# Performance work log

Hardware: AMD Instinct MI355X
Metric: run time of the kernel (lower is better)

The kernel has to match this reference:

```python
import jax, jax.numpy as jnp
import numpy as np

N = 100000
E = 3200000
NEG_SLOPE = 0.2


def setup_inputs() -> dict:
    key = jax.random.key(0)
    ks = jax.random.split(key, 12)
    x = jax.random.normal(ks[0], (N, 4), dtype=jnp.float32)
    edge_index = jax.random.randint(ks[1], (2, E), 0, N, dtype=jnp.int64)
    # GATConv(4, 16, heads=4): lin (no bias), att_src/att_dst [H, C], bias [H*C]
    W1 = jax.random.normal(ks[2], (4, 4 * 16), dtype=jnp.float32) * 0.5
    as1 = jax.random.normal(ks[3], (4, 16), dtype=jnp.float32) * 0.5
    ad1 = jax.random.normal(ks[4], (4, 16), dtype=jnp.float32) * 0.5
    b1 = jnp.zeros((64,), dtype=jnp.float32)
    # GATConv(64, 2, heads=4)
    W2 = jax.random.normal(ks[5], (64, 4 * 2), dtype=jnp.float32) * 0.125
    as2 = jax.random.normal(ks[6], (4, 2), dtype=jnp.float32) * 0.5
    ad2 = jax.random.normal(ks[7], (4, 2), dtype=jnp.float32) * 0.5
    b2 = jnp.zeros((8,), dtype=jnp.float32)
    # out head Linear(8, 1)
    Wout = jax.random.normal(ks[8], (8, 1), dtype=jnp.float32) * 0.35
    bout = jnp.zeros((1,), dtype=jnp.float32)
    return {"x": x, "edge_index": edge_index, "W1": W1, "as1": as1, "ad1": ad1,
            "b1": b1, "W2": W2, "as2": as2, "ad2": ad2, "b2": b2,
            "Wout": Wout, "bout": bout}


def gat_conv(x, ei, W, a_src, a_dst, b, H, C, n):
    # PyG GATConv (concat=True, negative_slope=0.2), self-loops already in ei
    xw = (x @ W).reshape(n, H, C)                      # [N, H, C]
    src, dst = ei[0], ei[1]
    alpha_s = jnp.einsum('nhc,hc->nh', xw, a_src)      # [N, H]
    alpha_d = jnp.einsum('nhc,hc->nh', xw, a_dst)      # [N, H]
    e = jax.nn.leaky_relu(alpha_s[src] + alpha_d[dst], NEG_SLOPE)  # [E, H]
    # segment softmax over incoming edges of each destination node
    m = jax.ops.segment_max(e, dst, num_segments=n)    # [N, H]
    e = jnp.exp(e - m[dst])
    denom = jax.ops.segment_sum(e, dst, num_segments=n)
    alpha = e / (denom[dst] + 1e-16)                   # [E, H]
    msg = xw[src] * alpha[:, :, None]                  # [E, H, C]
    out = jax.ops.segment_sum(msg, dst, num_segments=n)  # [N, H, C]
    return out.reshape(n, H * C) + b


def reference(x, edge_index, W1, as1, ad1, b1, W2, as2, ad2, b2, Wout, bout):
    n = x.shape[0]
    ar = jnp.arange(n, dtype=edge_index.dtype)
    ei = jnp.concatenate([edge_index, jnp.stack([ar, ar])], axis=1)  # add self-loops
    h = jax.nn.elu(gat_conv(x, ei, W1, as1, ad1, b1, 4, 16, n))       # [N, 64]
    h = jax.nn.elu(gat_conv(h, ei, W2, as2, ad2, b2, 4, 2, n))        # [N, 8]
    g = jnp.mean(h, axis=0, keepdims=True)  # global_mean_pool, batch all zeros -> [1, 8]
    return jax.nn.sigmoid(g @ Wout + bout)  # [1, 1]
```

## Files before the change

kernel.cpp:

```cpp
#include <hip/hip_runtime.h>
#include <hip/hip_fp8.h>

#define NEG 0.2f
#define BSZ 224
#define MAXBUK 512
#define NBIN 512

typedef float v2f __attribute__((ext_vector_type(2)));

__device__ __forceinline__ float lrelu(float x){ return fmaxf(x, NEG * x); }
__device__ __forceinline__ float elufast(float x){ return x > 0.0f ? x : __expf(x) - 1.0f; }
__device__ __forceinline__ float b2f(unsigned short b){ return __uint_as_float((unsigned)b << 16); }
__device__ __forceinline__ unsigned short f2b(float x){
    unsigned u = __float_as_uint(x);
    return (unsigned short)((u + 0x7FFFu + ((u >> 16) & 1u)) >> 16);
}

__device__ __forceinline__ void fma8(uint2 r, float w, v2f* acc){
    v2f w2 = {w, w};
    v2f f0 = __builtin_amdgcn_cvt_pk_f32_fp8(r.x, false);
    v2f f1 = __builtin_amdgcn_cvt_pk_f32_fp8(r.x, true);
    v2f f2 = __builtin_amdgcn_cvt_pk_f32_fp8(r.y, false);
    v2f f3 = __builtin_amdgcn_cvt_pk_f32_fp8(r.y, true);
    acc[0] = __builtin_elementwise_fma(f0, w2, acc[0]);
    acc[1] = __builtin_elementwise_fma(f1, w2, acc[1]);
    acc[2] = __builtin_elementwise_fma(f2, w2, acc[2]);
    acc[3] = __builtin_elementwise_fma(f3, w2, acc[3]);
}

__global__ void k_l1_node(const float* __restrict__ x, const float* __restrict__ W1,
                          const float* __restrict__ as1, const float* __restrict__ ad1,
                          unsigned char* __restrict__ xw1, uint2* __restrict__ asvb,
                          float* __restrict__ adv, int N){
    __shared__ float sW[256], sA[64], sD[64];
    int tid = threadIdx.x;
    sW[tid] = W1[tid];
    if (tid < 64){ sA[tid] = as1[tid]; sD[tid] = ad1[tid]; }
    __syncthreads();
    int i = blockIdx.x * 256 + tid;
    if (i >= N) return;
    float4 xv = ((const float4*)x)[i];
    float xw[64];
    #pragma unroll
    for (int j = 0; j < 64; j++)
        xw[j] = xv.x * sW[j] + xv.y * sW[64 + j] + xv.z * sW[128 + j] + xv.w * sW[192 + j];
    unsigned wv[16];
    #pragma unroll
    for (int j = 0; j < 16; j++){
        unsigned p = 0;
        p = __builtin_amdgcn_cvt_pk_fp8_f32(xw[4 * j],     xw[4 * j + 1], p, false);
        p = __builtin_amdgcn_cvt_pk_fp8_f32(xw[4 * j + 2], xw[4 * j + 3], p, true);
        wv[j] = p;
    }
    uint4* dp = (uint4*)(xw1 + (size_t)i * 64);
    dp[0] = make_uint4(wv[0],  wv[1],  wv[2],  wv[3]);
    dp[1] = make_uint4(wv[4],  wv[5],  wv[6],  wv[7]);
    dp[2] = make_uint4(wv[8],  wv[9],  wv[10], wv[11]);
    dp[3] = make_uint4(wv[12], wv[13], wv[14], wv[15]);
    float al[4];
    #pragma unroll
    for (int h = 0; h < 4; h++){
        float as_ = 0.f, ad_ = 0.f;
        #pragma unroll
        for (int c = 0; c < 16; c++){
            as_ += xw[h * 16 + c] * sA[h * 16 + c];
            ad_ += xw[h * 16 + c] * sD[h * 16 + c];
        }
        al[h] = as_;
        adv[i * 4 + h] = ad_;
    }
    asvb[i] = make_uint2((unsigned)f2b(al[0]) | ((unsigned)f2b(al[1]) << 16),
                         (unsigned)f2b(al[2]) | ((unsigned)f2b(al[3]) << 16));
}

__global__ void k_bcount(const int* __restrict__ dst, int* __restrict__ blkcnt,
                         int E, int chunksz, int nbuk){
    __shared__ int hist[MAXBUK];
    for (int b = threadIdx.x; b < nbuk; b += 256) hist[b] = 0;
    __syncthreads();
    int e0 = blockIdx.x * chunksz, e1 = min(E, e0 + chunksz);
    for (int e = e0 + threadIdx.x; e < e1; e += 256)
        atomicAdd(&hist[(unsigned)dst[e] / BSZ], 1);
    __syncthreads();
    for (int b = threadIdx.x; b < nbuk; b += 256)
        blkcnt[b * NBIN + blockIdx.x] = hist[b];
}

__global__ void k_scanA(int* __restrict__ blkcnt, int* __restrict__ btot){
    __shared__ int ts[256];
    int b = blockIdx.x, t = threadIdx.x;
    int base = b * NBIN + t * 2;
    int a0 = blkcnt[base], a1 = blkcnt[base + 1];
    int sum = a0 + a1;
    ts[t] = sum; __syncthreads();
    for (int s = 1; s < 256; s <<= 1){
        int tmp = (t >= s) ? ts[t - s] : 0;
        __syncthreads();
        ts[t] += tmp;
        __syncthreads();
    }
    int excl = ts[t] - sum;
    blkcnt[base] = excl;
    blkcnt[base + 1] = excl + a0;
    if (t == 255) btot[b] = ts[255];
}

__global__ void k_scanB(const int* __restrict__ btot, int* __restrict__ bstart, int nbuk){
    __shared__ int ts[512];
    int t = threadIdx.x;
    int v = (t < nbuk) ? btot[t] : 0;
    int orig = v;
    ts[t] = v; __syncthreads();
    for (int s = 1; s < 512; s <<= 1){
        int tmp = (t >= s) ? ts[t - s] : 0;
        __syncthreads();
        ts[t] += tmp;
        __syncthreads();
    }
    if (t < nbuk) bstart[t] = ts[t] - orig;
    if (t == 511) bstart[nbuk] = ts[511];
}

__global__ void k_bin(const int* __restrict__ src, const int* __restrict__ dst,
                      const int* __restrict__ blkcnt, const int* __restrict__ bstart,
                      unsigned* __restrict__ staged, int E, int chunksz, int nbuk){
    __shared__ int cur[MAXBUK];
    for (int b = threadIdx.x; b < nbuk; b += 256)
        cur[b] = bstart[b] + blkcnt[b * NBIN + blockIdx.x];
    __syncthreads();
    int e0 = blockIdx.x * chunksz, e1 = min(E, e0 + chunksz);
    for (int e = e0 + threadIdx.x; e < e1; e += 256){
        int d = dst[e];
        int buk = (unsigned)d / BSZ;
        int pos = atomicAdd(&cur[buk], 1);
        staged[pos] = (unsigned)src[e] | ((unsigned)(d - buk * BSZ) << 17);
    }
}

__global__ void k_local(const int* __restrict__ bstart, const unsigned* __restrict__ staged,
                        int* __restrict__ offp, int* __restrict__ csr, int N){
    __shared__ int deg[BSZ];
    __shared__ int cur[BSZ];
    __shared__ int ts[256];
    int b = blockIdx.x, t = threadIdx.x;
    int lo = b * BSZ, hi = min(N, lo + BSZ);
    int e0 = bstart[b], e1 = bstart[b + 1];
    if (t < BSZ) deg[t] = 0;
    __syncthreads();
    for (int e = e0 + t; e < e1; e += 256)
        atomicAdd(&deg[staged[e] >> 17], 1);
    __syncthreads();
    int v = (t < BSZ) ? deg[t] : 0;
    ts[t] = v; __syncthreads();
    for (int s = 1; s < 256; s <<= 1){
        int tmp = (t >= s) ? ts[t - s] : 0;
        __syncthreads();
        ts[t] += tmp;
        __syncthreads();
    }
    if (t < BSZ){
        cur[t] = e0 + ts[t] - v;
        if (lo + t < hi) offp[lo + t] = e0 + ts[t];
    }
    __syncthreads();
    for (int e = e0 + t; e < e1; e += 256){
        unsigned se = staged[e];
        int pos = atomicAdd(&cur[se >> 17], 1);
        csr[pos] = (int)(se & 0x1FFFFu);
    }
}

__global__ void k_l1_gather(const int* __restrict__ off, const int* __restrict__ csr,
                            const uint2* __restrict__ asvb, const float* __restrict__ adv,
                            const unsigned char* __restrict__ xw1, const float* __restrict__ b1,
                            unsigned char* __restrict__ h1f8, int N){
    int tid = threadIdx.x;
    int wid = (int)(((long)blockIdx.x * 256 + tid) >> 6);
    if (wid >= N) return;
    int lane = tid & 63;
    int g = lane >> 3;
    int q = lane & 7;
    int h = q >> 1;
    float advd = adv[wid * 4 + h];
    const unsigned char* xwq = xw1 + q * 8;
    const char* asvbh = (const char*)asvb + h * 2;

    v2f acc2[4] = {{0.f, 0.f}, {0.f, 0.f}, {0.f, 0.f}, {0.f, 0.f}};
    float den = 0.f;
    int k = wid ? off[wid - 1] : 0;
    int end = off[wid];
    for (; k + 16 <= end; k += 16){
        int sA = csr[k + g];
        int sB = csr[k + 8 + g];
        uint2 rA = *(const uint2*)(xwq + ((size_t)sA << 6));
        uint2 rB = *(const uint2*)(xwq + ((size_t)sB << 6));
        float aA = b2f(*(const unsigned short*)(asvbh + ((size_t)sA << 3)));
        float aB = b2f(*(const unsigned short*)(asvbh + ((size_t)sB << 3)));
        float tA = aA + advd, tB = aB + advd;
        float wA = __expf(fmaxf(tA, NEG * tA));
        float wB = __expf(fmaxf(tB, NEG * tB));
        den += wA + wB;
        fma8(rA, wA, acc2);
        fma8(rB, wB, acc2);
    }
    for (; k < end; k += 8){
        int e = k + g;
        bool valid = e < end;
        int s = csr[valid ? e : end - 1];
        uint2 r = *(const uint2*)(xwq + ((size_t)s << 6));
        float a = b2f(*(const unsigned short*)(asvbh + ((size_t)s << 3)));
        float t = a + advd;
        float w = valid ? __expf(fmaxf(t, NEG * t)) : 0.f;
        den += w;
        fma8(r, w, acc2);
    }
    #pragma unroll
    for (int m = 8; m <= 32; m <<= 1){
        #pragma unroll
        for (int j = 0; j < 4; j++){
            acc2[j].x += __shfl_xor(acc2[j].x, m);
            acc2[j].y += __shfl_xor(acc2[j].y, m);
        }
        den += __shfl_xor(den, m);
    }
    int c = q * 8 + g;
    float aself = b2f(*(const unsigned short*)(asvbh + ((size_t)wid << 3)));
    float tsv = aself + advd;
    float ws = __expf(fmaxf(tsv, NEG * tsv));
    unsigned selfb = xw1[(size_t)wid * 64 + c];
    v2f sf = __builtin_amdgcn_cvt_pk_f32_fp8(selfb, false);
    v2f tlo = (g & 2) ? acc2[1] : acc2[0];
    v2f thi = (g & 2) ? acc2[3] : acc2[2];
    v2f tt  = (g & 4) ? thi : tlo;
    float asel = ((g & 1) ? tt.y : tt.x) + ws * sf.x;
    float inv = 1.0f / (den + ws + 1e-16f);
    float o = elufast(asel * inv + b1[c]);
    unsigned p = __builtin_amdgcn_cvt_pk_fp8_f32(o, o, 0, false);
    h1f8[(size_t)wid * 64 + c] = (unsigned char)p;
}

__global__ void k_l2_node(const unsigned char* __restrict__ h1f8, const float* __restrict__ W2,
                          const float* __restrict__ ad2, float* __restrict__ xw2,
                          float* __restrict__ adv2, int N){
    __shared__ float sW[512], sD[8];
    int tid = threadIdx.x;
    sW[tid] = W2[tid];
    sW[256 + tid] = W2[256 + tid];
    if (tid < 8) sD[tid] = ad2[tid];
    __syncthreads();
    int i = blockIdx.x * 256 + tid;
    if (i >= N) return;
    const uint2* rp = (const uint2*)(h1f8 + (size_t)i * 64);
    float acc[8] = {0.f, 0.f, 0.f, 0.f, 0.f, 0.f, 0.f, 0.f};
    #pragma unroll
    for (int b8 = 0; b8 < 8; b8++){
        uint2 r = rp[b8];
        v2f f0 = __builtin_amdgcn_cvt_pk_f32_fp8(r.x, false);
        v2f f1 = __builtin_amdgcn_cvt_pk_f32_fp8(r.x, true);
        v2f f2 = __builtin_amdgcn_cvt_pk_f32_fp8(r.y, false);
        v2f f3 = __builtin_amdgcn_cvt_pk_f32_fp8(r.y, true);
        float f[8] = {f0.x, f0.y, f1.x, f1.y, f2.x, f2.y, f3.x, f3.y};
        #pragma unroll
        for (int j = 0; j < 8; j++){
            float hc = f[j];
            const float* wrow = &sW[(b8 * 8 + j) * 8];
            #pragma unroll
            for (int cc = 0; cc < 8; cc++) acc[cc] += hc * wrow[cc];
        }
    }
    float4* xo = (float4*)(xw2 + (size_t)i * 8);
    xo[0] = make_float4(acc[0], acc[1], acc[2], acc[3]);
    xo[1] = make_float4(acc[4], acc[5], acc[6], acc[7]);
    float4 dv;
    dv.x = acc[0] * sD[0] + acc[1] * sD[1];
    dv.y = acc[2] * sD[2] + acc[3] * sD[3];
    dv.z = acc[4] * sD[4] + acc[5] * sD[5];
    dv.w = acc[6] * sD[6] + acc[7] * sD[7];
    *(float4*)(adv2 + (size_t)i * 4) = dv;
}

__global__ void k_l2_gather(const int* __restrict__ off, const int* __restrict__ csr,
                            const float* __restrict__ adv2, const float* __restrict__ xw2,
                            const float* __restrict__ b2, const float* __restrict__ as2,
                            float* __restrict__ pool, int N){
    __shared__ float lpool[8];
    int tid = threadIdx.x;
    if (tid < 8) lpool[tid] = 0.f;
    __syncthreads();
    int wid = (int)(((long)blockIdx.x * 256 + tid) >> 6);
    if (wid < N){
        int lane = tid & 63;
        int g = lane >> 2;
        int hh = lane & 3;
        float2 a2h = *(const float2*)&as2[hh * 2];
        float advd = adv2[wid * 4 + hh];
        const char* xwh = (const char*)xw2 + hh * 8;
        v2f accv = {0.f, 0.f};
        float den = 0.f;

        auto edge = [&](int s, bool valid){
            v2f v = *(const v2f*)(xwh + ((size_t)s << 5));
            float al = v.x * a2h.x + v.y * a2h.y;
            float t = al + advd;
            float w = valid ? __expf(fmaxf(t, NEG * t)) : 0.f;
            den += w;
            v2f w2 = {w, w};
            accv = __builtin_elementwise_fma(v, w2, accv);
        };

        int k = wid ? off[wid - 1] : 0;
        int end = off[wid];
        for (; k + 32 <= end; k += 32){
            int s0 = csr[k + g], s1 = csr[k + 16 + g];
            edge(s0, true); edge(s1, true);
        }
        for (; k < end; k += 16){
            int e = k + g;
            bool valid = e < end;
            int s = csr[valid ? e : end - 1];
            edge(s, valid);
        }
        #pragma unroll
        for (int m = 4; m <= 32; m <<= 1){
            accv.x += __shfl_xor(accv.x, m);
            accv.y += __shfl_xor(accv.y, m);
            den    += __shfl_xor(den, m);
        }
        if (g == 0){
            v2f v = *(const v2f*)(xwh + ((size_t)wid << 5));
            float al = v.x * a2h.x + v.y * a2h.y;
            float t = al + advd;
            float ws = __expf(fmaxf(t, NEG * t));
            den += ws;
            accv.x += ws * v.x;
            accv.y += ws * v.y;
            float inv = 1.0f / (den + 1e-16f);
            float o0 = elufast(accv.x * inv + b2[hh * 2]);
            float o1 = elufast(accv.y * inv + b2[hh * 2 + 1]);
            atomicAdd(&lpool[hh * 2], o0);
            atomicAdd(&lpool[hh * 2 + 1], o1);
        }
    }
    __syncthreads();
    if (tid < 8) atomicAdd(&pool[(blockIdx.x & 63) * 8 + tid], lpool[tid]);
}

__global__ void k_final(const float* __restrict__ pool, const float* __restrict__ Wout,
                        const float* __restrict__ bout, float* __restrict__ out, float invN){
    int lane = threadIdx.x;
    const float4* p4 = (const float4*)(pool + lane * 8);
    float4 a = p4[0], b = p4[1];
    float v[8] = {a.x, a.y, a.z, a.w, b.x, b.y, b.z, b.w};
    #pragma unroll
    for (int m = 1; m <= 32; m <<= 1){
        #pragma unroll
        for (int j = 0; j < 8; j++) v[j] += __shfl_xor(v[j], m);
    }
    if (lane == 0){
        float z = bout[0];
        #pragma unroll
        for (int j = 0; j < 8; j++) z += v[j] * invN * Wout[j];
        out[0] = 1.0f / (1.0f + __expf(-z));
    }
}

extern "C" void kernel_launch(void* const* d_in, const int* in_sizes, int n_in,
                              void* d_out, int out_size, void* d_ws, size_t ws_size,
                              hipStream_t stream){
    const float* x    = (const float*)d_in[0];
    const int*   ei   = (const int*)d_in[1];
    const float* W1   = (const float*)d_in[2];
    const float* as1  = (const float*)d_in[3];
    const float* ad1  = (const float*)d_in[4];
    const float* b1   = (const float*)d_in[5];
    const float* W2   = (const float*)d_in[6];
    const float* as2  = (const float*)d_in[7];
    const float* ad2  = (const float*)d_in[8];
    const float* b2   = (const float*)d_in[9];
    const float* Wout = (const float*)d_in[10];
    const float* bout = (const float*)d_in[11];
    float* out = (float*)d_out;

    int N = in_sizes[0] / 4;
    int E = in_sizes[1] / 2;
    const int* src = ei;
    const int* dst = ei + E;

    char* ws = (char*)d_ws;
    size_t off_b = 0;
    auto alloc = [&](size_t bytes)->void*{
        void* p = ws + off_b;
        off_b += (bytes + 255) & ~(size_t)255;
        return p;
    };
    unsigned char* xw1  = (unsigned char*)alloc((size_t)N * 64);
    unsigned char* h1f8 = (unsigned char*)alloc((size_t)N * 64);
    uint2*    asvb   = (uint2*)alloc((size_t)N * 8);
    float*    adv    = (float*)alloc((size_t)N * 4 * 4);
    float*    adv2   = (float*)alloc((size_t)N * 4 * 4);
    int*      blkcnt = (int*)alloc((size_t)MAXBUK * NBIN * 4);
    int*      btot   = (int*)alloc((size_t)MAXBUK * 4);
    int*      bstart = (int*)alloc((size_t)(MAXBUK + 1) * 4);
    unsigned* staged = (unsigned*)alloc((size_t)E * 4);
    int*      offp   = (int*)alloc((size_t)N * 4);
    int*      csr    = (int*)alloc((size_t)E * 4);
    float*    xw2    = (float*)alloc((size_t)N * 8 * 4);
    float*    pool   = (float*)alloc(64 * 8 * 4);

    int nbuk = (N + BSZ - 1) / BSZ;
    int chunksz = (E + NBIN - 1) / NBIN;

    hipMemsetAsync(pool, 0, 64 * 8 * 4, stream);

    k_bcount<<<NBIN, 256, 0, stream>>>(dst, blkcnt, E, chunksz, nbuk);
    k_l1_node<<<(N + 255) / 256, 256, 0, stream>>>(x, W1, as1, ad1, xw1, asvb, adv, N);
    k_scanA<<<nbuk, 256, 0, stream>>>(blkcnt, btot);
    k_scanB<<<1, 512, 0, stream>>>(btot, bstart, nbuk);
    k_bin<<<NBIN, 256, 0, stream>>>(src, dst, blkcnt, bstart, staged, E, chunksz, nbuk);
    k_local<<<nbuk, 256, 0, stream>>>(bstart, staged, offp, csr, N);

    k_l1_gather<<<(int)(((long)N * 64 + 255) / 256), 256, 0, stream>>>(
        offp, csr, asvb, adv, xw1, b1, h1f8, N);
    k_l2_node<<<(N + 255) / 256, 256, 0, stream>>>(h1f8, W2, ad2, xw2, adv2, N);
    k_l2_gather<<<(int)(((long)N * 64 + 255) / 256), 256, 0, stream>>>(
        offp, csr, adv2, xw2, b2, as2, pool, N);
    k_final<<<1, 64, 0, stream>>>(pool, Wout, bout, out, 1.0f / (float)N);
}
```

Baseline: 188.5 us.

## Add nontemporal memory hints, dual accumulators and transpose-style wave reduction

Marks streaming loads and stores (edge lists, staged buffers, CSR, fp8 features) as nontemporal so they do not pollute cache. The layer-1 gather loop is unrolled to 32 edges per iteration with two independent accumulator sets to expose more memory-level parallelism, and the same dual-accumulator split is applied to layer 2. The layer-1 cross-lane reduction becomes a butterfly transpose that cuts the number of shuffles needed. The risk is that nontemporal hints on data reused by later kernels (csr, xw1 in L2) may raise DRAM traffic, and the extra accumulators add register pressure.

```diff
diff --git a/kernel.cpp b/kernel.cpp
--- a/kernel.cpp
+++ b/kernel.cpp
@@ -7,8 +7,9 @@
 #define NBIN 512
 
 typedef float v2f __attribute__((ext_vector_type(2)));
-
-__device__ __forceinline__ float lrelu(float x){ return fmaxf(x, NEG * x); }
+typedef unsigned u32x2 __attribute__((ext_vector_type(2)));
+typedef unsigned u32x4 __attribute__((ext_vector_type(4)));
+
 __device__ __forceinline__ float elufast(float x){ return x > 0.0f ? x : __expf(x) - 1.0f; }
 __device__ __forceinline__ float b2f(unsigned short b){ return __uint_as_float((unsigned)b << 16); }
 __device__ __forceinline__ unsigned short f2b(float x){
@@ -52,11 +53,15 @@
         p = __builtin_amdgcn_cvt_pk_fp8_f32(xw[4 * j + 2], xw[4 * j + 3], p, true);
         wv[j] = p;
     }
-    uint4* dp = (uint4*)(xw1 + (size_t)i * 64);
-    dp[0] = make_uint4(wv[0],  wv[1],  wv[2],  wv[3]);
-    dp[1] = make_uint4(wv[4],  wv[5],  wv[6],  wv[7]);
-    dp[2] = make_uint4(wv[8],  wv[9],  wv[10], wv[11]);
-    dp[3] = make_uint4(wv[12], wv[13], wv[14], wv[15]);
+    u32x4* dp = (u32x4*)(xw1 + (size_t)i * 64);
+    u32x4 q0 = {wv[0],  wv[1],  wv[2],  wv[3]};
+    u32x4 q1 = {wv[4],  wv[5],  wv[6],  wv[7]};
+    u32x4 q2 = {wv[8],  wv[9],  wv[10], wv[11]};
+    u32x4 q3 = {wv[12], wv[13], wv[14], wv[15]};
+    __builtin_nontemporal_store(q0, dp + 0);
+    __builtin_nontemporal_store(q1, dp + 1);
+    __builtin_nontemporal_store(q2, dp + 2);
+    __builtin_nontemporal_store(q3, dp + 3);
     float al[4];
     #pragma unroll
     for (int h = 0; h < 4; h++){
@@ -80,7 +85,7 @@
     __syncthreads();
     int e0 = blockIdx.x * chunksz, e1 = min(E, e0 + chunksz);
     for (int e = e0 + threadIdx.x; e < e1; e += 256)
-        atomicAdd(&hist[(unsigned)dst[e] / BSZ], 1);
+        atomicAdd(&hist[(unsigned)__builtin_nontemporal_load(dst + e) / BSZ], 1);
     __syncthreads();
     for (int b = threadIdx.x; b < nbuk; b += 256)
         blkcnt[b * NBIN + blockIdx.x] = hist[b];
@@ -130,10 +135,12 @@
     __syncthreads();
     int e0 = blockIdx.x * chunksz, e1 = min(E, e0 + chunksz);
     for (int e = e0 + threadIdx.x; e < e1; e += 256){
-        int d = dst[e];
+        int d = __builtin_nontemporal_load(dst + e);
+        int s = __builtin_nontemporal_load(src + e);
         int buk = (unsigned)d / BSZ;
         int pos = atomicAdd(&cur[buk], 1);
-        staged[pos] = (unsigned)src[e] | ((unsigned)(d - buk * BSZ) << 17);
+        __builtin_nontemporal_store((unsigned)s | ((unsigned)(d - buk * BSZ) << 17),
+                                    staged + pos);
     }
 }
 
@@ -164,9 +171,9 @@
     }
     __syncthreads();
     for (int e = e0 + t; e < e1; e += 256){
-        unsigned se = staged[e];
+        unsigned se = __builtin_nontemporal_load(staged + e);
         int pos = atomicAdd(&cur[se >> 17], 1);
-        csr[pos] = (int)(se & 0x1FFFFu);
+        __builtin_nontemporal_store((int)(se & 0x1FFFFu), csr + pos);
     }
 }
 
@@ -185,58 +192,85 @@
     const unsigned char* xwq = xw1 + q * 8;
     const char* asvbh = (const char*)asvb + h * 2;
 
-    v2f acc2[4] = {{0.f, 0.f}, {0.f, 0.f}, {0.f, 0.f}, {0.f, 0.f}};
-    float den = 0.f;
+    v2f accA[4] = {{0.f,0.f},{0.f,0.f},{0.f,0.f},{0.f,0.f}};
+    v2f accB[4] = {{0.f,0.f},{0.f,0.f},{0.f,0.f},{0.f,0.f}};
+    float denA = 0.f, denB = 0.f;
+
+    auto edge = [&](int s, v2f* acc, float& dn){
+        uint2 r = *(const uint2*)(xwq + ((size_t)s << 6));
+        float a = b2f(*(const unsigned short*)(asvbh + ((size_t)s << 3)));
+        float t = a + advd;
+        float w = __expf(fmaxf(t, NEG * t));
+        dn += w;
+        fma8(r, w, acc);
+    };
+
     int k = wid ? off[wid - 1] : 0;
     int end = off[wid];
-    for (; k + 16 <= end; k += 16){
-        int sA = csr[k + g];
-        int sB = csr[k + 8 + g];
-        uint2 rA = *(const uint2*)(xwq + ((size_t)sA << 6));
-        uint2 rB = *(const uint2*)(xwq + ((size_t)sB << 6));
-        float aA = b2f(*(const unsigned short*)(asvbh + ((size_t)sA << 3)));
-        float aB = b2f(*(const unsigned short*)(asvbh + ((size_t)sB << 3)));
-        float tA = aA + advd, tB = aB + advd;
-        float wA = __expf(fmaxf(tA, NEG * tA));
-        float wB = __expf(fmaxf(tB, NEG * tB));
-        den += wA + wB;
-        fma8(rA, wA, acc2);
-        fma8(rB, wB, acc2);
+    for (; k + 32 <= end; k += 32){
+        int s0 = __builtin_nontemporal_load(csr + k + g);
+        int s1 = __builtin_nontemporal_load(csr + k + 8 + g);
+        int s2 = __builtin_nontemporal_load(csr + k + 16 + g);
+        int s3 = __builtin_nontemporal_load(csr + k + 24 + g);
+        edge(s0, accA, denA); edge(s1, accB, denB);
+        edge(s2, accA, denA); edge(s3, accB, denB);
+    }
+    if (k + 16 <= end){
+        int s0 = __builtin_nontemporal_load(csr + k + g);
+        int s1 = __builtin_nontemporal_load(csr + k + 8 + g);
+        edge(s0, accA, denA); edge(s1, accB, denB);
+        k += 16;
     }
     for (; k < end; k += 8){
         int e = k + g;
         bool valid = e < end;
-        int s = csr[valid ? e : end - 1];
+        int s = __builtin_nontemporal_load(csr + (valid ? e : end - 1));
         uint2 r = *(const uint2*)(xwq + ((size_t)s << 6));
         float a = b2f(*(const unsigned short*)(asvbh + ((size_t)s << 3)));
         float t = a + advd;
         float w = valid ? __expf(fmaxf(t, NEG * t)) : 0.f;
-        den += w;
-        fma8(r, w, acc2);
-    }
-    #pragma unroll
-    for (int m = 8; m <= 32; m <<= 1){
-        #pragma unroll
-        for (int j = 0; j < 4; j++){
-            acc2[j].x += __shfl_xor(acc2[j].x, m);
-            acc2[j].y += __shfl_xor(acc2[j].y, m);
-        }
-        den += __shfl_xor(den, m);
-    }
+        denA += w;
+        fma8(r, w, accA);
+    }
+    v2f a0 = accA[0] + accB[0];
+    v2f a1 = accA[1] + accB[1];
+    v2f a2 = accA[2] + accB[2];
+    v2f a3 = accA[3] + accB[3];
+    float den = denA + denB;
+
+    v2f t0, t1, t2, t3;
+    t0.x = __shfl_xor(a0.x, 32); t0.y = __shfl_xor(a0.y, 32);
+    t1.x = __shfl_xor(a1.x, 32); t1.y = __shfl_xor(a1.y, 32);
+    t2.x = __shfl_xor(a2.x, 32); t2.y = __shfl_xor(a2.y, 32);
+    t3.x = __shfl_xor(a3.x, 32); t3.y = __shfl_xor(a3.y, 32);
+    bool gb2 = (lane & 32) != 0;
+    v2f n0 = gb2 ? (a2 + t2) : (a0 + t0);
+    v2f n1 = gb2 ? (a3 + t3) : (a1 + t1);
+    v2f u0, u1;
+    u0.x = __shfl_xor(n0.x, 16); u0.y = __shfl_xor(n0.y, 16);
+    u1.x = __shfl_xor(n1.x, 16); u1.y = __shfl_xor(n1.y, 16);
+    bool gb1 = (lane & 16) != 0;
+    v2f rr = gb1 ? (n1 + u1) : (n0 + u0);
+    v2f z;
+    z.x = __shfl_xor(rr.x, 8); z.y = __shfl_xor(rr.y, 8);
+    rr += z;
+    bool gb0 = (lane & 8) != 0;
+    den += __shfl_xor(den, 8);
+    den += __shfl_xor(den, 16);
+    den += __shfl_xor(den, 32);
+    float val = gb0 ? rr.y : rr.x;
+
     int c = q * 8 + g;
     float aself = b2f(*(const unsigned short*)(asvbh + ((size_t)wid << 3)));
     float tsv = aself + advd;
     float ws = __expf(fmaxf(tsv, NEG * tsv));
     unsigned selfb = xw1[(size_t)wid * 64 + c];
     v2f sf = __builtin_amdgcn_cvt_pk_f32_fp8(selfb, false);
-    v2f tlo = (g & 2) ? acc2[1] : acc2[0];
-    v2f thi = (g & 2) ? acc2[3] : acc2[2];
-    v2f tt  = (g & 4) ? thi : tlo;
-    float asel = ((g & 1) ? tt.y : tt.x) + ws * sf.x;
+    float asel = val + ws * sf.x;
     float inv = 1.0f / (den + ws + 1e-16f);
     float o = elufast(asel * inv + b1[c]);
     unsigned p = __builtin_amdgcn_cvt_pk_fp8_f32(o, o, 0, false);
-    h1f8[(size_t)wid * 64 + c] = (unsigned char)p;
+    __builtin_nontemporal_store((unsigned char)p, h1f8 + (size_t)wid * 64 + c);
 }
 
 __global__ void k_l2_node(const unsigned char* __restrict__ h1f8, const float* __restrict__ W2,
@@ -250,11 +284,11 @@
     __syncthreads();
     int i = blockIdx.x * 256 + tid;
     if (i >= N) return;
-    const uint2* rp = (const uint2*)(h1f8 + (size_t)i * 64);
+    const u32x2* rp = (const u32x2*)(h1f8 + (size_t)i * 64);
     float acc[8] = {0.f, 0.f, 0.f, 0.f, 0.f, 0.f, 0.f, 0.f};
     #pragma unroll
     for (int b8 = 0; b8 < 8; b8++){
-        uint2 r = rp[b8];
+        u32x2 r = __builtin_nontemporal_load(rp + b8);
         v2f f0 = __builtin_amdgcn_cvt_pk_f32_fp8(r.x, false);
         v2f f1 = __builtin_amdgcn_cvt_pk_f32_fp8(r.x, true);
         v2f f2 = __builtin_amdgcn_cvt_pk_f32_fp8(r.y, false);
@@ -295,31 +329,34 @@
         float2 a2h = *(const float2*)&as2[hh * 2];
         float advd = adv2[wid * 4 + hh];
         const char* xwh = (const char*)xw2 + hh * 8;
-        v2f accv = {0.f, 0.f};
-        float den = 0.f;
-
-        auto edge = [&](int s, bool valid){
+        v2f accA = {0.f, 0.f}, accB = {0.f, 0.f};
+        float denA = 0.f, denB = 0.f;
+
+        auto edge = [&](int s, bool valid, v2f& acc, float& dn){
             v2f v = *(const v2f*)(xwh + ((size_t)s << 5));
             float al = v.x * a2h.x + v.y * a2h.y;
             float t = al + advd;
             float w = valid ? __expf(fmaxf(t, NEG * t)) : 0.f;
-            den += w;
+            dn += w;
             v2f w2 = {w, w};
-            accv = __builtin_elementwise_fma(v, w2, accv);
+            acc = __builtin_elementwise_fma(v, w2, acc);
         };
 
         int k = wid ? off[wid - 1] : 0;
         int end = off[wid];
         for (; k + 32 <= end; k += 32){
-            int s0 = csr[k + g], s1 = csr[k + 16 + g];
-            edge(s0, true); edge(s1, true);
+            int s0 = __builtin_nontemporal_load(csr + k + g);
+            int s1 = __builtin_nontemporal_load(csr + k + 16 + g);
+            edge(s0, true, accA, denA); edge(s1, true, accB, denB);
         }
         for (; k < end; k += 16){
             int e = k + g;
             bool valid = e < end;
-            int s = csr[valid ? e : end - 1];
-            edge(s, valid);
-        }
+            int s = __builtin_nontemporal_load(csr + (valid ? e : end - 1));
+            edge(s, valid, accA, denA);
+        }
+        v2f accv = accA + accB;
+        float den = denA + denB;
         #pragma unroll
         for (int m = 4; m <= 32; m <<= 1){
             accv.x += __shfl_xor(accv.x, m);
```

New measurement: 371.6 us. 97.2% more time.
